# Optimization experiments

Measured on AMD Instinct MI355X. Metric: run time of the kernel, lower is better.

Reference implementation:

```python
import math
import jax
import jax.numpy as jnp
import numpy as np

DIM = 1024
NUM_EXPERTS = 4
CAPACITY = (0.25, 0.25, 0.25, 0.25)
BATCH = 8
NUM_TOKENS = 4096


def setup_inputs() -> dict:
    key = jax.random.key(0)
    k1, k2 = jax.random.split(key)
    input_tokens = jax.random.normal(k1, (BATCH, NUM_TOKENS, DIM), dtype=jnp.float32)
    # torch Linear weight [out_features, in_features], init uniform(-0.02, 0.02), bias zeros
    W = jax.random.uniform(k2, (NUM_EXPERTS, DIM), dtype=jnp.float32, minval=-0.02, maxval=0.02)
    b = jnp.zeros((NUM_EXPERTS,), dtype=jnp.float32)
    return {"input_tokens": input_tokens, "W": W, "b": b}


def reference(input_tokens, W, b):
    # router probs in float32 (autocast disabled in original)
    logits = jnp.einsum('bnd,ed->bne', input_tokens, W) + b  # [B, N, E]
    probs = jax.nn.softmax(logits, axis=-1)

    B, N, _ = probs.shape
    token_mask = jnp.full((B, N), -1, dtype=jnp.int32)
    neg_inf = jnp.float32(-jnp.inf)

    # Sequential expert-preferred assignment, highest expert index first.
    for j in reversed(range(NUM_EXPERTS)):
        capacity = int(math.floor(CAPACITY[j] * N))
        if capacity == 0:
            continue
        r_j = jnp.where(token_mask != -1, neg_inf, probs[:, :, j])  # mask already-assigned tokens
        _, topk_idx = jax.lax.top_k(r_j, capacity)  # [B, capacity]
        # Faithful to torch `token_mask[:, topk_indices] = j`: assigns expert j at the
        # union of selected token positions across ALL batch rows (broadcast over dim 0).
        token_mask = token_mask.at[:, topk_idx.reshape(-1)].set(j)

    token_mask = jnp.where(token_mask == -1, 0, token_mask)
    expert_probs = jnp.take_along_axis(probs, token_mask[..., None], axis=2)[..., 0]  # [B, N]
    return token_mask, expert_probs
```

## Files before the change

kernel.cpp:

```cpp
#include <hip/hip_runtime.h>
#include <math.h>

#define DIM 1024
#define NE 4
#define NTOK 4096
#define NB 8
#define CAP 1024

__global__ __launch_bounds__(256) void probs_kernel(const float* __restrict__ tokens,
                                                    const float* __restrict__ W,
                                                    const float* __restrict__ bias,
                                                    float* __restrict__ probs,
                                                    unsigned* __restrict__ counter) {
    __shared__ float4 Wl[NE * 256];
    int tid = threadIdx.x;
    if (blockIdx.x == 0 && tid == 0) counter[0] = 0u;
    const float4* W4 = (const float4*)W;
    for (int i = tid; i < NE * 256; i += 256) Wl[i] = W4[i];
    __syncthreads();

    int wave = tid >> 6, lane = tid & 63;
    long tok = (long)blockIdx.x * 4 + wave;
    const float4* t4 = (const float4*)(tokens + tok * DIM);

    double a0 = 0, a1 = 0, a2 = 0, a3 = 0;
#pragma unroll
    for (int kk = 0; kk < 4; kk++) {
        int c = lane + 64 * kk;
        float4 v  = t4[c];
        float4 w0 = Wl[0 * 256 + c];
        float4 w1 = Wl[1 * 256 + c];
        float4 w2 = Wl[2 * 256 + c];
        float4 w3 = Wl[3 * 256 + c];
        a0 += (double)v.x * w0.x + (double)v.y * w0.y + (double)v.z * w0.z + (double)v.w * w0.w;
        a1 += (double)v.x * w1.x + (double)v.y * w1.y + (double)v.z * w1.z + (double)v.w * w1.w;
        a2 += (double)v.x * w2.x + (double)v.y * w2.y + (double)v.z * w2.z + (double)v.w * w2.w;
        a3 += (double)v.x * w3.x + (double)v.y * w3.y + (double)v.z * w3.z + (double)v.w * w3.w;
    }
#pragma unroll
    for (int off = 32; off > 0; off >>= 1) {
        a0 += __shfl_xor(a0, off);
        a1 += __shfl_xor(a1, off);
        a2 += __shfl_xor(a2, off);
        a3 += __shfl_xor(a3, off);
    }
    if (lane == 0) {
        float f0 = (float)(a0 + (double)bias[0]);
        float f1 = (float)(a1 + (double)bias[1]);
        float f2 = (float)(a2 + (double)bias[2]);
        float f3 = (float)(a3 + (double)bias[3]);
        double m = fmax(fmax((double)f0, (double)f1), fmax((double)f2, (double)f3));
        double e0 = exp((double)f0 - m);
        double e1 = exp((double)f1 - m);
        double e2 = exp((double)f2 - m);
        double e3 = exp((double)f3 - m);
        double s = e0 + e1 + e2 + e3;
        float4 p;
        p.x = (float)(e0 / s);
        p.y = (float)(e1 / s);
        p.z = (float)(e2 / s);
        p.w = (float)(e3 / s);
        ((float4*)probs)[tok] = p;
    }
}


__device__ __forceinline__ unsigned block_exscan_1024(unsigned v, unsigned* wl,
                                                      int tid, unsigned* total) {
    int lane = tid & 63, w = tid >> 6;
    unsigned s = v;
#pragma unroll
    for (int off = 1; off < 64; off <<= 1) {
        unsigned t = __shfl_up(s, off);
        if (lane >= off) s += t;
    }
    if (lane == 63) wl[w] = s;
    __syncthreads();
    if (tid < 64) {
        unsigned x = (tid < 16) ? wl[tid] : 0u;
#pragma unroll
        for (int off = 1; off < 16; off <<= 1) {
            unsigned t = __shfl_up(x, off);
            if (lane >= off) x += t;
        }
        if (tid < 16) wl[tid] = x;
    }
    __syncthreads();
    unsigned waveoff = (w == 0) ? 0u : wl[w - 1];
    unsigned tot = wl[15];
    __syncthreads();
    if (total) *total = tot;
    return waveoff + (s - v);
}

__device__ __forceinline__ void radix_select_regs(const unsigned key[4], unsigned cap,
                                                  unsigned* hist, unsigned* scanb,
                                                  unsigned* bcast, int tid,
                                                  unsigned* v_out, unsigned* rem_out) {
    if (tid == 0) { bcast[0] = 0u; bcast[1] = cap; }
    __syncthreads();
#pragma unroll
    for (int shift = 24; shift >= 0; shift -= 8) {
        if (tid < 256) hist[tid] = 0u;
        __syncthreads();
        unsigned pref = bcast[0], rem = bcast[1];
        bool all = (shift == 24);
#pragma unroll
        for (int k = 0; k < 4; k++) {
            if (all || (key[k] >> (shift + 8)) == pref)
                atomicAdd(&hist[(key[k] >> shift) & 255u], 1u);
        }
        __syncthreads();
        if (tid < 64) {
            unsigned h0 = hist[4 * tid], h1 = hist[4 * tid + 1];
            unsigned h2 = hist[4 * tid + 2], h3 = hist[4 * tid + 3];
            unsigned s3 = h3, s2 = h2 + s3, s1 = h1 + s2, s0 = h0 + s1;
            unsigned t = s0, s = t;
#pragma unroll
            for (int off = 1; off < 64; off <<= 1) {
                unsigned o = __shfl_down(s, off);
                if (tid + off < 64) s += o;
            }
            unsigned E = s - t;
            scanb[4 * tid]     = E + s0;
            scanb[4 * tid + 1] = E + s1;
            scanb[4 * tid + 2] = E + s2;
            scanb[4 * tid + 3] = E + s3;
        }
        __syncthreads();
        if (tid < 256) {
            unsigned incl = scanb[tid];
            unsigned excl = (tid < 255) ? scanb[tid + 1] : 0u;
            if (excl < rem && rem <= incl) {
                bcast[0] = (pref << 8) | (unsigned)tid;
                bcast[1] = rem - excl;
            }
        }
        __syncthreads();
    }
    *v_out = bcast[0];
    *rem_out = bcast[1];
}

__device__ __forceinline__ unsigned mono_key(float p) {
    unsigned bits = __float_as_uint(p);
    return (bits & 0x80000000u) ? ~bits : (bits | 0x80000000u);
}

__device__ __forceinline__ void select_to_bitmap(const unsigned key[4], unsigned* bitmap,
                                                 unsigned* hist, unsigned* scanb,
                                                 unsigned* bcast, unsigned* wl, int tid) {
    unsigned vstar, rem;
    radix_select_regs(key, CAP, hist, scanb, bcast, tid, &vstar, &rem);
    unsigned loc[4], v = 0;
#pragma unroll
    for (int k = 0; k < 4; k++) { loc[k] = (key[k] == vstar); v += loc[k]; }
    unsigned tot;
    unsigned ex = block_exscan_1024(v, wl, tid, &tot);
#pragma unroll
    for (int k = 0; k < 4; k++) {
        int i = 4 * tid + k;
        bool sel = (key[k] > vstar) || (loc[k] && ex < rem);
        ex += loc[k];
        if (sel) atomicOr(&bitmap[i >> 5], 1u << (i & 31));
    }
    __syncthreads();
}

__global__ __launch_bounds__(1024) void selrest_kernel(const float* __restrict__ probs,
                                                       unsigned* __restrict__ selbits,
                                                       unsigned* __restrict__ counter,
                                                       int* __restrict__ finalmask) {
    __shared__ int maskv[NTOK];
    __shared__ unsigned hist[256], scanb[256], bcast[2];
    __shared__ unsigned bitmap[128];
    __shared__ unsigned wl[17];
    __shared__ int islast;
    int b = blockIdx.x, tid = threadIdx.x;

    const float4* p4 = (const float4*)probs + (size_t)b * NTOK;
    unsigned key[4];
#pragma unroll
    for (int k = 0; k < 4; k++) key[k] = mono_key(p4[4 * tid + k].w);
    if (tid < 128) bitmap[tid] = 0u;
    __syncthreads();

    select_to_bitmap(key, bitmap, hist, scanb, bcast, wl, tid);

    if (tid < 128) atomicExch(&selbits[b * 128 + tid], bitmap[tid]);
    __threadfence();
    __syncthreads();
    if (tid == 0) islast = (atomicAdd(counter, 1u) == NB - 1);
    __syncthreads();
    if (!islast) return;

    __threadfence();
    if (tid < 128) {
        unsigned u = 0;
#pragma unroll
        for (int bb = 0; bb < NB; bb++) u |= atomicOr(&selbits[bb * 128 + tid], 0u);
        bitmap[tid] = u;
    }
    __syncthreads();
#pragma unroll
    for (int k = 0; k < 4; k++) {
        int i = tid + k * 1024;
        maskv[i] = ((bitmap[i >> 5] >> (i & 31)) & 1u) ? 3 : -1;
    }
    __syncthreads();

    for (int j = 2; j >= 0; j--) {
        unsigned loc[4], v = 0;
#pragma unroll
        for (int k = 0; k < 4; k++) { loc[k] = (maskv[4 * tid + k] != -1); v += loc[k]; }
        unsigned M;
        unsigned ex = block_exscan_1024(v, wl, tid, &M);
        unsigned U = NTOK - M;

        if (U <= CAP) {
            unsigned need = CAP - U;
#pragma unroll
            for (int k = 0; k < 4; k++) {
                int i = 4 * tid + k;
                bool sel = (!loc[k]) || (ex < need);
                ex += loc[k];
                if (sel) maskv[i] = j;
            }
            __syncthreads();
        } else {
            if (tid < 128) bitmap[tid] = 0u;
            __syncthreads();
            for (int bb = 0; bb < NB; bb++) {
                unsigned k2[4];
#pragma unroll
                for (int k = 0; k < 4; k++) {
                    int i = 4 * tid + k;
                    k2[k] = (maskv[i] != -1)
                                ? 0u
                                : mono_key(probs[((size_t)bb * NTOK + i) * NE + j]);
                }
                select_to_bitmap(k2, bitmap, hist, scanb, bcast, wl, tid);
            }
#pragma unroll
            for (int k = 0; k < 4; k++) {
                int i = 4 * tid + k;
                if ((bitmap[i >> 5] >> (i & 31)) & 1u) maskv[i] = j;
            }
            __syncthreads();
        }
    }

#pragma unroll
    for (int k = 0; k < 4; k++) {
        int i = tid + k * 1024;
        int m = maskv[i];
        finalmask[i] = (m < 0) ? 0 : m;
    }
}

__global__ __launch_bounds__(256) void final_kernel(const float* __restrict__ probs,
                                                    const int* __restrict__ fm,
                                                    float* __restrict__ out) {
    int i = blockIdx.x * 256 + threadIdx.x;
    int n = i & (NTOK - 1);
    int m = fm[n];
    out[i] = (float)m;
    out[NB * NTOK + i] = probs[(size_t)i * NE + m];
}

extern "C" void kernel_launch(void* const* d_in, const int* in_sizes, int n_in,
                              void* d_out, int out_size, void* d_ws, size_t ws_size,
                              hipStream_t stream) {
    const float* tokens = (const float*)d_in[0];
    const float* W      = (const float*)d_in[1];
    const float* bias   = (const float*)d_in[2];
    float* out = (float*)d_out;

    float*    probs   = (float*)d_ws;
    unsigned* selbits = (unsigned*)((char*)d_ws + (size_t)NB * NTOK * NE * sizeof(float));
    int*      fmask   = (int*)(selbits + NB * 128);
    unsigned* counter = (unsigned*)(fmask + NTOK);

    probs_kernel<<<(NB * NTOK) / 4, 256, 0, stream>>>(tokens, W, bias, probs, counter);
    selrest_kernel<<<NB, 1024, 0, stream>>>(probs, selbits, counter, fmask);
    final_kernel<<<(NB * NTOK) / 256, 256, 0, stream>>>(probs, fmask, out);
}
```

Measured before the change: 214.4 us.

## Split selection into separate kernels, use per-wave radix histograms, nontemporal token loads

The fused select/rest kernel with its atomic last-block counter is split into two kernels (per-batch expert-3 selection, then a single-block remaining-expert pass), so the global atomics and threadfences go away. The radix select now builds per-wave padded histograms that are summed afterwards, which reduces shared-memory atomic contention. Token loads in the probs kernel use nontemporal loads to avoid polluting the cache. The cost is one extra kernel launch and a small extra reduction step per radix pass.

Measured after the change: 211.4 us. About the same (-1.4%).

```diff
diff --git a/kernel.cpp b/kernel.cpp
--- a/kernel.cpp
+++ b/kernel.cpp
@@ -6,28 +6,30 @@
 #define NTOK 4096
 #define NB 8
 #define CAP 1024
+#define NWAVE 16
+#define HSTRIDE 257
+
+typedef float fx4 __attribute__((ext_vector_type(4)));
 
 __global__ __launch_bounds__(256) void probs_kernel(const float* __restrict__ tokens,
                                                     const float* __restrict__ W,
                                                     const float* __restrict__ bias,
-                                                    float* __restrict__ probs,
-                                                    unsigned* __restrict__ counter) {
+                                                    float* __restrict__ probs) {
     __shared__ float4 Wl[NE * 256];
     int tid = threadIdx.x;
-    if (blockIdx.x == 0 && tid == 0) counter[0] = 0u;
     const float4* W4 = (const float4*)W;
     for (int i = tid; i < NE * 256; i += 256) Wl[i] = W4[i];
     __syncthreads();
 
     int wave = tid >> 6, lane = tid & 63;
     long tok = (long)blockIdx.x * 4 + wave;
-    const float4* t4 = (const float4*)(tokens + tok * DIM);
+    const fx4* t4 = (const fx4*)(tokens + tok * DIM);
 
     double a0 = 0, a1 = 0, a2 = 0, a3 = 0;
 #pragma unroll
     for (int kk = 0; kk < 4; kk++) {
         int c = lane + 64 * kk;
-        float4 v  = t4[c];
+        fx4 v = __builtin_nontemporal_load(&t4[c]);
         float4 w0 = Wl[0 * 256 + c];
         float4 w1 = Wl[1 * 256 + c];
         float4 w2 = Wl[2 * 256 + c];
@@ -94,21 +96,30 @@
 }
 
 __device__ __forceinline__ void radix_select_regs(const unsigned key[4], unsigned cap,
-                                                  unsigned* hist, unsigned* scanb,
-                                                  unsigned* bcast, int tid,
+                                                  unsigned* whist, unsigned* hist,
+                                                  unsigned* scanb, unsigned* bcast,
+                                                  int tid,
                                                   unsigned* v_out, unsigned* rem_out) {
+    int w = tid >> 6;
+    unsigned* myh = whist + w * HSTRIDE;
     if (tid == 0) { bcast[0] = 0u; bcast[1] = cap; }
-    __syncthreads();
 #pragma unroll
     for (int shift = 24; shift >= 0; shift -= 8) {
-        if (tid < 256) hist[tid] = 0u;
+        for (int i = tid; i < NWAVE * HSTRIDE; i += 1024) whist[i] = 0u;
         __syncthreads();
         unsigned pref = bcast[0], rem = bcast[1];
         bool all = (shift == 24);
 #pragma unroll
         for (int k = 0; k < 4; k++) {
             if (all || (key[k] >> (shift + 8)) == pref)
-                atomicAdd(&hist[(key[k] >> shift) & 255u], 1u);
+                atomicAdd(&myh[(key[k] >> shift) & 255u], 1u);
+        }
+        __syncthreads();
+        if (tid < 256) {
+            unsigned s = 0;
+#pragma unroll
+            for (int w2 = 0; w2 < NWAVE; w2++) s += whist[w2 * HSTRIDE + tid];
+            hist[tid] = s;
         }
         __syncthreads();
         if (tid < 64) {
@@ -148,10 +159,11 @@
 }
 
 __device__ __forceinline__ void select_to_bitmap(const unsigned key[4], unsigned* bitmap,
-                                                 unsigned* hist, unsigned* scanb,
-                                                 unsigned* bcast, unsigned* wl, int tid) {
+                                                 unsigned* whist, unsigned* hist,
+                                                 unsigned* scanb, unsigned* bcast,
+                                                 unsigned* wl, int tid) {
     unsigned vstar, rem;
-    radix_select_regs(key, CAP, hist, scanb, bcast, tid, &vstar, &rem);
+    radix_select_regs(key, CAP, whist, hist, scanb, bcast, tid, &vstar, &rem);
     unsigned loc[4], v = 0;
 #pragma unroll
     for (int k = 0; k < 4; k++) { loc[k] = (key[k] == vstar); v += loc[k]; }
@@ -167,15 +179,12 @@
     __syncthreads();
 }
 
-__global__ __launch_bounds__(1024) void selrest_kernel(const float* __restrict__ probs,
-                                                       unsigned* __restrict__ selbits,
-                                                       unsigned* __restrict__ counter,
-                                                       int* __restrict__ finalmask) {
-    __shared__ int maskv[NTOK];
+__global__ __launch_bounds__(1024) void select3_kernel(const float* __restrict__ probs,
+                                                       unsigned* __restrict__ selbits) {
+    __shared__ unsigned whist[NWAVE * HSTRIDE];
     __shared__ unsigned hist[256], scanb[256], bcast[2];
     __shared__ unsigned bitmap[128];
     __shared__ unsigned wl[17];
-    __shared__ int islast;
     int b = blockIdx.x, tid = threadIdx.x;
 
     const float4* p4 = (const float4*)probs + (size_t)b * NTOK;
@@ -183,22 +192,26 @@
 #pragma unroll
     for (int k = 0; k < 4; k++) key[k] = mono_key(p4[4 * tid + k].w);
     if (tid < 128) bitmap[tid] = 0u;
-    __syncthreads();
-
-    select_to_bitmap(key, bitmap, hist, scanb, bcast, wl, tid);
-
-    if (tid < 128) atomicExch(&selbits[b * 128 + tid], bitmap[tid]);
-    __threadfence();
-    __syncthreads();
-    if (tid == 0) islast = (atomicAdd(counter, 1u) == NB - 1);
-    __syncthreads();
-    if (!islast) return;
-
-    __threadfence();
+
+    select_to_bitmap(key, bitmap, whist, hist, scanb, bcast, wl, tid);
+
+    if (tid < 128) selbits[b * 128 + tid] = bitmap[tid];
+}
+
+__global__ __launch_bounds__(1024) void rest_kernel(const float* __restrict__ probs,
+                                                    const unsigned* __restrict__ selbits,
+                                                    int* __restrict__ finalmask) {
+    __shared__ int maskv[NTOK];
+    __shared__ unsigned whist[NWAVE * HSTRIDE];
+    __shared__ unsigned hist[256], scanb[256], bcast[2];
+    __shared__ unsigned bitmap[128];
+    __shared__ unsigned wl[17];
+    int tid = threadIdx.x;
+
     if (tid < 128) {
         unsigned u = 0;
 #pragma unroll
-        for (int bb = 0; bb < NB; bb++) u |= atomicOr(&selbits[bb * 128 + tid], 0u);
+        for (int bb = 0; bb < NB; bb++) u |= selbits[bb * 128 + tid];
         bitmap[tid] = u;
     }
     __syncthreads();
@@ -239,7 +252,7 @@
                                 ? 0u
                                 : mono_key(probs[((size_t)bb * NTOK + i) * NE + j]);
                 }
-                select_to_bitmap(k2, bitmap, hist, scanb, bcast, wl, tid);
+                select_to_bitmap(k2, bitmap, whist, hist, scanb, bcast, wl, tid);
             }
 #pragma unroll
             for (int k = 0; k < 4; k++) {
@@ -279,9 +292,9 @@
     float*    probs   = (float*)d_ws;
     unsigned* selbits = (unsigned*)((char*)d_ws + (size_t)NB * NTOK * NE * sizeof(float));
     int*      fmask   = (int*)(selbits + NB * 128);
-    unsigned* counter = (unsigned*)(fmask + NTOK);
-
-    probs_kernel<<<(NB * NTOK) / 4, 256, 0, stream>>>(tokens, W, bias, probs, counter);
-    selrest_kernel<<<NB, 1024, 0, stream>>>(probs, selbits, counter, fmask);
+
+    probs_kernel<<<(NB * NTOK) / 4, 256, 0, stream>>>(tokens, W, bias, probs);
+    select3_kernel<<<NB, 1024, 0, stream>>>(probs, selbits);
+    rest_kernel<<<1, 1024, 0, stream>>>(probs, selbits, fmask);
     final_kernel<<<(NB * NTOK) / 256, 256, 0, stream>>>(probs, fmask, out);
 }
```
